# Performance work log

Measured on AMD Instinct MI355X. Metric: run time of the kernel, lower is better.

The kernel has to match this reference:

```python
import jax, jax.numpy as jnp
import numpy as np

T, B, E, H = 2048, 2, 1024, 16
DH = E // H
SCALE = DH ** -0.5
NEG = jnp.finfo(jnp.float32).min


def setup_inputs() -> dict:
    key = jax.random.key(0)
    ks = jax.random.split(key, 10)
    s = 0.02
    query = jax.random.normal(ks[0], (T, B, E), dtype=jnp.float32)
    key_padding_mask = jax.random.randint(ks[1], (B, T), 0, 2).astype(bool)
    # causal additive mask, broadcastable over (bsz, heads, tgt, src)
    causal = jnp.triu(jnp.ones((T, T), dtype=bool), k=1)
    attn_mask = jnp.where(causal, NEG, 0.0).astype(jnp.float32)[None, None]
    Wq = jax.random.normal(ks[2], (E, E), jnp.float32) * s
    bq = jax.random.normal(ks[3], (E,), jnp.float32) * s
    Wk = jax.random.normal(ks[4], (E, E), jnp.float32) * s
    bk = jax.random.normal(ks[5], (E,), jnp.float32) * s
    Wv = jax.random.normal(ks[6], (E, E), jnp.float32) * s
    bv = jax.random.normal(ks[7], (E,), jnp.float32) * s
    Wo = jax.random.normal(ks[8], (E, E), jnp.float32) * s
    bo = jax.random.normal(ks[9], (E,), jnp.float32) * s
    return {"query": query, "key_padding_mask": key_padding_mask, "attn_mask": attn_mask,
            "Wq": Wq, "bq": bq, "Wk": Wk, "bk": bk, "Wv": Wv, "bv": bv, "Wo": Wo, "bo": bo}


def _heads(x):
    # [T, B, E] -> [B, H, T, DH]
    return x.reshape(T, B, H, DH).transpose(1, 2, 0, 3)


def reference(query, key_padding_mask, attn_mask, Wq, bq, Wk, bk, Wv, bv, Wo, bo):
    # projections (torch Linear: x @ W.T + b); q scaled as in module
    q = _heads((query @ Wq.T + bq) * SCALE)          # [B,H,T,DH]
    k = _heads(query @ Wk.T + bk)                    # [B,H,S,DH] (self-attn: S=T)
    v = _heads(query @ Wv.T + bv)
    scores = jnp.einsum('bhtd,bhsd->bhts', q, k)     # [B,H,T,S]
    scores = scores + attn_mask                      # additive causal mask
    # key_padding_mask True -> masked_fill with dtype min
    scores = jnp.where(key_padding_mask[:, None, None, :], NEG, scores)
    probs = jax.nn.softmax(scores, axis=-1)
    ctx = jnp.einsum('bhts,bhsd->bhtd', probs, v)    # [B,H,T,DH]
    ctx = ctx.transpose(2, 0, 1, 3).reshape(T, B, E) # back to [T,B,E]
    return ctx @ Wo.T + bo
```

## Files before the change

kernel.cpp:

```cpp
#include <hip/hip_runtime.h>
#include <hip/hip_bf16.h>
#include <stdint.h>

typedef unsigned short u16;
typedef uint32_t u32;
typedef unsigned long long u64;
typedef __attribute__((ext_vector_type(8))) short bf16x8;
typedef __attribute__((ext_vector_type(4))) float f32x4;
typedef __attribute__((ext_vector_type(16))) float f32x16;
typedef __attribute__((ext_vector_type(4))) u32 u32x4;

#define T_SEQ 2048

__device__ __forceinline__ float bf2f(u16 u) {
  union { u32 i; float f; } v; v.i = ((u32)u) << 16; return v.f;
}
__device__ __forceinline__ u16 f2bf(float f) {
  union { float f; u32 i; } v; v.f = f;
  u32 u = v.i;
  return (u16)((u + 0x7fffu + ((u >> 16) & 1u)) >> 16);
}

#if __has_builtin(__builtin_amdgcn_exp2f)
#define EXP2F(x) __builtin_amdgcn_exp2f(x)
#else
#define EXP2F(x) exp2f(x)
#endif

__device__ __forceinline__ u32 permpack(float lo, float hi) {
#if __has_builtin(__builtin_amdgcn_perm)
  return __builtin_amdgcn_perm(__float_as_uint(hi), __float_as_uint(lo), 0x07060302u);
#else
  return (__float_as_uint(hi) & 0xFFFF0000u) | (__float_as_uint(lo) >> 16);
#endif
}

__device__ __forceinline__ void gload_lds16(const void* g, void* l) {
  __builtin_amdgcn_global_load_lds(
      (const __attribute__((address_space(1))) void*)g,
      (__attribute__((address_space(3))) void*)l, 16, 0, 0);
}

__global__ __launch_bounds__(256) void cvt_kernel(const float* __restrict__ src,
                                                  u16* __restrict__ dst, int n) {
  int i = (blockIdx.x * 256 + threadIdx.x) * 4;
  if (i + 3 < n) {
    const float4 v = *(const float4*)(src + i);
    ushort4 o;
    o.x = f2bf(v.x); o.y = f2bf(v.y); o.z = f2bf(v.z); o.w = f2bf(v.w);
    *(ushort4*)(dst + i) = o;
  }
}

__global__ __launch_bounds__(256) void cvt4_kernel(
    const float* __restrict__ s0, const float* __restrict__ s1,
    const float* __restrict__ s2, const float* __restrict__ s3,
    u16* __restrict__ dst) {
  const int z = blockIdx.y;
  const float* src = (z == 0) ? s0 : (z == 1) ? s1 : (z == 2) ? s2 : s3;
  int i = (blockIdx.x * 256 + threadIdx.x) * 4;
  const float4 v = *(const float4*)(src + i);
  ushort4 o;
  o.x = f2bf(v.x); o.y = f2bf(v.y); o.z = f2bf(v.z); o.w = f2bf(v.w);
  *(ushort4*)(dst + (size_t)z * 1048576 + i) = o;
}

__device__ __forceinline__ void gemm_core_128x128(
    f32x4 acc[2][4], const u16* __restrict__ A, const u16* __restrict__ Bw,
    int bm, int bn, u16* As, u16* Bs)
{
  const int tid = threadIdx.x;
  const int w = tid >> 6, lane = tid & 63, g = lane >> 4, c = lane & 15;
  const int wr = (w & 3) * 32, wc = (w >> 2) * 64;
  for (int k0 = 0; k0 < 1024; k0 += 64) {
    __syncthreads();
    #pragma unroll
    for (int is = 0; is < 2; ++is) {
      int o = (is*8 + w)*1024 + lane*16;
      int row = o >> 7, c16 = (o >> 4) & 7;
      gload_lds16(A + (size_t)(bm*128 + row)*1024 + k0 + (c16 ^ (row & 7))*8,
                  (char*)As + (is*8 + w)*1024);
    }
    #pragma unroll
    for (int is = 0; is < 2; ++is) {
      int o = (is*8 + w)*1024 + lane*16;
      int row = o >> 7, c16 = (o >> 4) & 7;
      gload_lds16(Bw + (size_t)(bn*128 + row)*1024 + k0 + (c16 ^ (row & 7))*8,
                  (char*)Bs + (is*8 + w)*1024);
    }
    __syncthreads();
    bf16x8 af[2][2], bfr[4][2];
    #pragma unroll
    for (int mf = 0; mf < 2; ++mf)
      #pragma unroll
      for (int kc = 0; kc < 2; ++kc) {
        int row = wr + mf*16 + c;
        int colb = kc*64 + g*16;
        af[mf][kc] = *(const bf16x8*)((const char*)As + row*128 + (colb ^ ((row & 7) << 4)));
      }
    #pragma unroll
    for (int nf = 0; nf < 4; ++nf)
      #pragma unroll
      for (int kc = 0; kc < 2; ++kc) {
        int row = wc + nf*16 + c;
        int colb = kc*64 + g*16;
        bfr[nf][kc] = *(const bf16x8*)((const char*)Bs + row*128 + (colb ^ ((row & 7) << 4)));
      }
    #pragma unroll
    for (int mf = 0; mf < 2; ++mf)
      #pragma unroll
      for (int nf = 0; nf < 4; ++nf)
        #pragma unroll
        for (int kc = 0; kc < 2; ++kc)
          acc[mf][nf] = __builtin_amdgcn_mfma_f32_16x16x32_bf16(
              af[mf][kc], bfr[nf][kc], acc[mf][nf], 0, 0, 0);
  }
}

__global__ __launch_bounds__(512, 2) void gemm_qkv(
    const u16* __restrict__ Abf, const u16* __restrict__ Wbf,
    const float* __restrict__ bq, const float* __restrict__ bk,
    const float* __restrict__ bv, u16* __restrict__ qkvh)
{
  __shared__ __align__(16) u16 As[128*64];
  __shared__ __align__(16) u16 Bs[128*64];
  f32x4 acc[2][4];
  #pragma unroll
  for (int mf = 0; mf < 2; ++mf)
    #pragma unroll
    for (int nf = 0; nf < 4; ++nf) acc[mf][nf] = (f32x4){0.f,0.f,0.f,0.f};
  const int z = blockIdx.z;
  gemm_core_128x128(acc, Abf, Wbf + (size_t)z*1048576, blockIdx.x, blockIdx.y, As, Bs);
  const float* bias = (z == 0) ? bq : (z == 1) ? bk : bv;
  const float scl = (z == 0) ? 0.18033688011112043f : 1.0f;
  u16* dst = qkvh + (size_t)z * 4194304;
  const int tid = threadIdx.x, w = tid >> 6, lane = tid & 63, g = lane >> 4, c = lane & 15;
  const int wr = (w & 3) * 32, wc = (w >> 2) * 64;
  #pragma unroll
  for (int mf = 0; mf < 2; ++mf)
    #pragma unroll
    for (int nf = 0; nf < 4; ++nf) {
      int col = blockIdx.y*128 + wc + nf*16 + c;
      float bcol = bias[col];
      int h = col >> 6, d = col & 63;
      #pragma unroll
      for (int r = 0; r < 4; ++r) {
        int row = blockIdx.x*128 + wr + mf*16 + g*4 + r;
        int t = row >> 1, bb = row & 1;
        float v = (acc[mf][nf][r] + bcol) * scl;
        dst[(size_t)(bb*16 + h)*131072 + (size_t)t*64 + d] = f2bf(v);
      }
    }
}

__global__ __launch_bounds__(512, 2) void gemm_out(
    const u16* __restrict__ ctx2, const u16* __restrict__ Wobf,
    const float* __restrict__ bo, float* __restrict__ out)
{
  __shared__ __align__(16) u16 As[128*64];
  __shared__ __align__(16) u16 Bs[128*64];
  f32x4 acc[2][4];
  #pragma unroll
  for (int mf = 0; mf < 2; ++mf)
    #pragma unroll
    for (int nf = 0; nf < 4; ++nf) acc[mf][nf] = (f32x4){0.f,0.f,0.f,0.f};
  gemm_core_128x128(acc, ctx2, Wobf, blockIdx.x, blockIdx.y, As, Bs);
  const int tid = threadIdx.x, w = tid >> 6, lane = tid & 63, g = lane >> 4, c = lane & 15;
  const int wr = (w & 3) * 32, wc = (w >> 2) * 64;
  #pragma unroll
  for (int mf = 0; mf < 2; ++mf)
    #pragma unroll
    for (int nf = 0; nf < 4; ++nf) {
      int col = blockIdx.y*128 + wc + nf*16 + c;
      float bcol = bo[col];
      #pragma unroll
      for (int r = 0; r < 4; ++r) {
        int row = blockIdx.x*128 + wr + mf*16 + g*4 + r;
        out[(size_t)row*1024 + col] = acc[mf][nf][r] + bcol;
      }
    }
}

__global__ __launch_bounds__(256) void vtrans_kernel(const u16* __restrict__ Vh,
                                                     u16* __restrict__ Vt,
                                                     float* __restrict__ vs) {
  __shared__ u16 tile[64][72];
  const int bh = blockIdx.x >> 5, tc = blockIdx.x & 31;
  const int t0 = tc * 64;
  const int tid = threadIdx.x;
  {
    const int tl = tid >> 2, d0 = (tid & 3) * 16;
    const u16* src = Vh + (size_t)bh*131072 + (size_t)(t0 + tl)*64 + d0;
    bf16x8 a = *(const bf16x8*)src;
    bf16x8 b2 = *(const bf16x8*)(src + 8);
    #pragma unroll
    for (int j = 0; j < 8; ++j) {
      tile[d0 + j][tl] = (u16)a[j];
      tile[d0 + 8 + j][tl] = (u16)b2[j];
    }
  }
  __syncthreads();
  {
    const int d = tid >> 2, tq = (tid & 3) * 16;
    bf16x8 o0, o1;
    float s = 0.f;
    #pragma unroll
    for (int j = 0; j < 8; ++j) {
      u16 x0 = tile[d][tq + j], x1 = tile[d][tq + 8 + j];
      o0[j] = (short)x0; o1[j] = (short)x1;
      s += bf2f(x0) + bf2f(x1);
    }
    u16* dst = Vt + (size_t)bh*131072 + (size_t)d*2048 + t0 + tq;
    *(bf16x8*)dst = o0;
    *(bf16x8*)(dst + 8) = o1;
    s += __shfl_xor(s, 1, 64);
    s += __shfl_xor(s, 2, 64);
    if ((tid & 3) == 0) atomicAdd(&vs[bh*64 + d], s);
  }
}

#define ZERO16 (f32x16){0.f,0.f,0.f,0.f,0.f,0.f,0.f,0.f,0.f,0.f,0.f,0.f,0.f,0.f,0.f,0.f}
#define NEGINF (-__builtin_inff())

__global__ __launch_bounds__(64, 2) void flash_attn(
    const u16* __restrict__ Qh, const u16* __restrict__ Kh,
    const u16* __restrict__ Vt, const int* __restrict__ kpm,
    const float* __restrict__ vsum, u16* __restrict__ ctx2,
    u16* __restrict__ pctx, float* __restrict__ pml)
{
  const int lane = threadIdx.x;
  const int l31 = lane & 31, hi = lane >> 5;

  const int id = blockIdx.x;
  const int xcd = id & 7, rest = id >> 3;
  const int bh = xcd * 4 + (rest & 3);
  const int pp = rest >> 2;
  int qt, ch, NS;
  if (pp < 32) { qt = pp; ch = 0; NS = 1; }
  else { int uu = pp - 32; qt = 32 + (uu >> 1); ch = uu & 1; NS = 2; }
  const int b = bh >> 4, h = bh & 15;
  const int q0 = qt * 32;
  const size_t hbase = (size_t)bh * 131072;
  const int nt = (qt >> 1) + 1;
  int lo, hicap;
  if (NS == 1) { lo = 0; hicap = nt; }
  else { int h1 = nt >> 1; lo = ch ? h1 : 0; hicap = ch ? nt : h1; }
  const int q = q0 + l31;

  bf16x8 qfrag[4];
  #pragma unroll
  for (int kt = 0; kt < 4; ++kt)
    qfrag[kt] = *(const bf16x8*)(Qh + hbase + (size_t)q*64 + kt*16 + hi*8);

  bf16x8 kreg[2][4];
  #pragma unroll
  for (int sub = 0; sub < 2; ++sub)
    #pragma unroll
    for (int kt = 0; kt < 4; ++kt)
      kreg[sub][kt] = *(const bf16x8*)(Kh + hbase + (size_t)(lo*64 + sub*32 + l31)*64 + kt*16 + hi*8);

  int kpmv_cur = kpm[b*T_SEQ + lo*64 + lane];
  int kpmv_nxt = 0;

  float mrow = NEGINF, lrow = 0.f;
  f32x16 cacc0 = ZERO16, cacc1 = ZERO16;

  for (int t = lo; t < hicap; ++t) {
    const int s0 = t * 64;
    const bool notLast = (t + 1 < hicap);
    const bool diag = (t == nt - 1);

    bf16x8 vf[2][4];
    #pragma unroll
    for (int db = 0; db < 2; ++db)
      #pragma unroll
      for (int ks = 0; ks < 4; ++ks)
        vf[db][ks] = *(const bf16x8*)(Vt + hbase + (size_t)(db*32 + l31)*2048 + s0 + ks*16 + hi*8);

    f32x16 st0 = ZERO16, st1 = ZERO16;
    __builtin_amdgcn_s_setprio(1);
    #pragma unroll
    for (int kt = 0; kt < 4; ++kt) {
      st0 = __builtin_amdgcn_mfma_f32_32x32x16_bf16(kreg[0][kt], qfrag[kt], st0, 0, 0, 0);
      st1 = __builtin_amdgcn_mfma_f32_32x32x16_bf16(kreg[1][kt], qfrag[kt], st1, 0, 0, 0);
    }
    __builtin_amdgcn_s_setprio(0);

    if (notLast) {
      #pragma unroll
      for (int sub = 0; sub < 2; ++sub)
        #pragma unroll
        for (int kt = 0; kt < 4; ++kt)
          kreg[sub][kt] = *(const bf16x8*)(Kh + hbase + (size_t)(s0 + 64 + sub*32 + l31)*64 + kt*16 + hi*8);
      kpmv_nxt = kpm[b*T_SEQ + s0 + 64 + lane];
    }

    {
      const u64 mask = __ballot(kpmv_cur != 0);
      const u32 m0 = (u32)mask, m1 = (u32)(mask >> 32);
      const u64 m4 = mask >> 4;
      const u32 m4l = (u32)m4, m4h = (u32)(m4 >> 32);
      const u32 w0 = hi ? m4l : m0;
      const u32 w1 = hi ? m4h : m1;
      const int lim = q - s0 - 4*hi;
      #pragma unroll
      for (int m = 0; m < 4; ++m) {
        u32 nib0 = (w0 >> (m*8)) & 15u;
        u32 nib1 = (w1 >> (m*8)) & 15u;
        if (diag) {
          int t0c = lim - m*8;       int c0 = min(max(t0c + 1, 0), 4);
          int t1c = lim - 32 - m*8;  int c1 = min(max(t1c + 1, 0), 4);
          nib0 |= (0xFu << c0) & 0xFu;
          nib1 |= (0xFu << c1) & 0xFu;
        }
        #pragma unroll
        for (int r = 0; r < 4; ++r) {
          if ((nib0 >> r) & 1) st0[m*4 + r] = NEGINF;
          if ((nib1 >> r) & 1) st1[m*4 + r] = NEGINF;
        }
      }
      float t8[8];
      #pragma unroll
      for (int i = 0; i < 8; ++i)
        t8[i] = fmaxf(fmaxf(st0[i], st0[i+8]), fmaxf(st1[i], st1[i+8]));
      float t4a = fmaxf(t8[0], t8[4]), t4b = fmaxf(t8[1], t8[5]);
      float t4c = fmaxf(t8[2], t8[6]), t4d = fmaxf(t8[3], t8[7]);
      float rm = fmaxf(fmaxf(t4a, t4b), fmaxf(t4c, t4d));
      rm = fmaxf(rm, __shfl_xor(rm, 32, 64));

      const bool need = (rm > mrow + 8.f) || (mrow < -1e30f);
      if (__any(need)) {
        const float mn = fmaxf(mrow, rm);
        const float sc = (mn < -1e30f) ? 1.f : EXP2F(mrow - mn);
        mrow = mn;
        lrow *= sc;
        #pragma unroll
        for (int i = 0; i < 16; ++i) { cacc0[i] *= sc; cacc1[i] *= sc; }
      }
      const bool dead = (mrow < -1e30f);
      float a0 = 0.f, a1 = 0.f, a2 = 0.f, a3 = 0.f;
      #pragma unroll
      for (int i = 0; i < 16; i += 4) {
        float p0 = dead ? 0.f : EXP2F(st0[i+0] - mrow); st0[i+0] = p0; a0 += p0;
        float p1 = dead ? 0.f : EXP2F(st0[i+1] - mrow); st0[i+1] = p1; a1 += p1;
        float p2 = dead ? 0.f : EXP2F(st0[i+2] - mrow); st0[i+2] = p2; a2 += p2;
        float p3 = dead ? 0.f : EXP2F(st0[i+3] - mrow); st0[i+3] = p3; a3 += p3;
      }
      #pragma unroll
      for (int i = 0; i < 16; i += 4) {
        float p0 = dead ? 0.f : EXP2F(st1[i+0] - mrow); st1[i+0] = p0; a0 += p0;
        float p1 = dead ? 0.f : EXP2F(st1[i+1] - mrow); st1[i+1] = p1; a1 += p1;
        float p2 = dead ? 0.f : EXP2F(st1[i+2] - mrow); st1[i+2] = p2; a2 += p2;
        float p3 = dead ? 0.f : EXP2F(st1[i+3] - mrow); st1[i+3] = p3; a3 += p3;
      }
      float ps = (a0 + a1) + (a2 + a3);
      ps += __shfl_xor(ps, 32, 64);
      lrow += ps;
    }

    u32 pk[8][2];
    #pragma unroll
    for (int m = 0; m < 4; ++m) {
      pk[m][0]   = permpack(st0[m*4+0], st0[m*4+1]);
      pk[m][1]   = permpack(st0[m*4+2], st0[m*4+3]);
      pk[4+m][0] = permpack(st1[m*4+0], st1[m*4+1]);
      pk[4+m][1] = permpack(st1[m*4+2], st1[m*4+3]);
    }
    bf16x8 pf[4];
    #pragma unroll
    for (int ks = 0; ks < 4; ++ks) {
      u32 own0 = pk[2*ks][0],   own1 = pk[2*ks][1];
      u32 oth0 = pk[2*ks+1][0], oth1 = pk[2*ks+1][1];
      u32 r0 = __shfl_xor(hi ? own0 : oth0, 32, 64);
      u32 r1 = __shfl_xor(hi ? own1 : oth1, 32, 64);
      u32 w0 = hi ? r0 : own0;
      u32 w1 = hi ? r1 : own1;
      u32 w2 = hi ? oth0 : r0;
      u32 w3 = hi ? oth1 : r1;
      u32x4 wv = {w0, w1, w2, w3};
      pf[ks] = __builtin_bit_cast(bf16x8, wv);
    }

    __builtin_amdgcn_s_setprio(1);
    #pragma unroll
    for (int ks = 0; ks < 4; ++ks)
      cacc0 = __builtin_amdgcn_mfma_f32_32x32x16_bf16(vf[0][ks], pf[ks], cacc0, 0, 0, 0);
    #pragma unroll
    for (int ks = 0; ks < 4; ++ks)
      cacc1 = __builtin_amdgcn_mfma_f32_32x32x16_bf16(vf[1][ks], pf[ks], cacc1, 0, 0, 0);
    __builtin_amdgcn_s_setprio(0);

    kpmv_cur = kpmv_nxt;
  }

  if (NS == 1) {
    const bool dead = (lrow == 0.f);
    const float rl = dead ? 0.f : 1.f / lrow;
    #pragma unroll
    for (int subd = 0; subd < 2; ++subd) {
      #pragma unroll
      for (int m = 0; m < 4; ++m) {
        const int d0 = subd*32 + hi*4 + m*8;
        float v0 = (subd ? cacc1[m*4+0] : cacc0[m*4+0]) * rl;
        float v1 = (subd ? cacc1[m*4+1] : cacc0[m*4+1]) * rl;
        float v2 = (subd ? cacc1[m*4+2] : cacc0[m*4+2]) * rl;
        float v3 = (subd ? cacc1[m*4+3] : cacc0[m*4+3]) * rl;
        if (dead) {
          const float* vs = vsum + bh*64 + d0;
          v0 = vs[0] * (1.0f/2048.0f);
          v1 = vs[1] * (1.0f/2048.0f);
          v2 = vs[2] * (1.0f/2048.0f);
          v3 = vs[3] * (1.0f/2048.0f);
        }
        ushort4 o;
        o.x = f2bf(v0); o.y = f2bf(v1); o.z = f2bf(v2); o.w = f2bf(v3);
        *(ushort4*)(ctx2 + (size_t)(q*2 + b)*1024 + h*64 + d0) = o;
      }
    }
  } else {
    const int slot = ((bh << 5) + (qt - 32))*2 + ch;
    u16* pc = pctx + (size_t)slot*2048 + (size_t)l31*64;
    #pragma unroll
    for (int subd = 0; subd < 2; ++subd) {
      #pragma unroll
      for (int m = 0; m < 4; ++m) {
        const int d0 = subd*32 + hi*4 + m*8;
        const f32x16& cc = subd ? cacc1 : cacc0;
        ushort4 o;
        o.x = f2bf(cc[m*4+0]); o.y = f2bf(cc[m*4+1]);
        o.z = f2bf(cc[m*4+2]); o.w = f2bf(cc[m*4+3]);
        *(ushort4*)(pc + d0) = o;
      }
    }
    if (!hi) {
      float2 ml; ml.x = mrow; ml.y = lrow;
      *(float2*)(pml + (size_t)slot*64 + l31*2) = ml;
    }
  }
}

__global__ __launch_bounds__(64) void combine_kernel(
    const u16* __restrict__ pctx, const float* __restrict__ pml,
    const float* __restrict__ vsum, u16* __restrict__ ctx2)
{
  const int qtm = blockIdx.x, bh = blockIdx.y;
  const int qt = 32 + qtm;
  const int b = bh >> 4, h = bh & 15;
  const int lane = threadIdx.x;
  const int qr = lane >> 1, d0 = (lane & 1) * 32;
  const int slot0 = ((bh << 5) + qtm)*2;
  const float* ml0 = pml + (size_t)slot0*64 + qr*2;
  const float* ml1 = pml + (size_t)(slot0+1)*64 + qr*2;
  const float m1 = ml0[0], l1 = ml0[1];
  const float m2 = ml1[0], l2 = ml1[1];
  const float ms = fmaxf(m1, m2);
  bool dead = (ms == NEGINF);
  const float w1 = dead ? 0.f : EXP2F(m1 - ms);
  const float w2 = dead ? 0.f : EXP2F(m2 - ms);
  const float lt = w1*l1 + w2*l2;
  dead = dead || (lt == 0.f);
  const float rl = dead ? 0.f : 1.f / lt;
  const u16* c1 = pctx + ((size_t)slot0*32 + qr)*64 + d0;
  const u16* c2 = pctx + ((size_t)(slot0+1)*32 + qr)*64 + d0;
  const int qrow = qt*32 + qr;
  u16* dst = ctx2 + (size_t)(qrow*2 + b)*1024 + h*64 + d0;
  #pragma unroll
  for (int g2 = 0; g2 < 4; ++g2) {
    bf16x8 a = *(const bf16x8*)(c1 + g2*8);
    bf16x8 bb = *(const bf16x8*)(c2 + g2*8);
    bf16x8 o;
    #pragma unroll
    for (int j = 0; j < 8; ++j) {
      float v = (w1*bf2f((u16)a[j]) + w2*bf2f((u16)bb[j])) * rl;
      if (dead) v = vsum[bh*64 + d0 + g2*8 + j] * (1.0f/2048.0f);
      o[j] = (short)f2bf(v);
    }
    *(bf16x8*)(dst + g2*8) = o;
  }
}

extern "C" void kernel_launch(void* const* d_in, const int* in_sizes, int n_in,
                              void* d_out, int out_size, void* d_ws, size_t ws_size,
                              hipStream_t stream) {
  const float* query = (const float*)d_in[0];
  const int*   kpm   = (const int*)d_in[1];
  const float* Wq = (const float*)d_in[3];
  const float* bq = (const float*)d_in[4];
  const float* Wk = (const float*)d_in[5];
  const float* bk = (const float*)d_in[6];
  const float* Wv = (const float*)d_in[7];
  const float* bv = (const float*)d_in[8];
  const float* Wo = (const float*)d_in[9];
  const float* bo = (const float*)d_in[10];

  char* ws = (char*)d_ws;
  u16*   qbf  = (u16*)(ws);
  u16*   Vt   = (u16*)(ws);
  u16*   wbf  = (u16*)(ws + 8388608);
  u16*   qkvh = (u16*)(ws + 16777216);
  u16*   pctx = (u16*)(ws + 33554432);
  u16*   ctx2 = (u16*)(ws + 41943040);
  float* vsum = (float*)(ws + 50331648);
  float* pml  = (float*)(ws + 50339840);

  cvt_kernel<<<dim3(4096), 256, 0, stream>>>(query, qbf, 4194304);
  cvt4_kernel<<<dim3(1024, 4), 256, 0, stream>>>(Wq, Wk, Wv, Wo, wbf);

  hipMemsetAsync(vsum, 0, 2048 * sizeof(float), stream);

  gemm_qkv<<<dim3(32, 8, 3), 512, 0, stream>>>(qbf, wbf, bq, bk, bv, qkvh);
  vtrans_kernel<<<dim3(1024), 256, 0, stream>>>(qkvh + 2*4194304, Vt, vsum);
  flash_attn<<<dim3(3072), 64, 0, stream>>>(qkvh, qkvh + 1*4194304,
                                            Vt, kpm, vsum, ctx2, pctx, pml);
  combine_kernel<<<dim3(32, 32), 64, 0, stream>>>(pctx, pml, vsum, ctx2);
  gemm_out<<<dim3(32, 8), 512, 0, stream>>>(ctx2, wbf + 3*1048576, bo, (float*)d_out);
}
```

Before: 152.2 us.

## Share K/V tiles via double-buffered LDS across two query waves in flash attention

Flash attention now runs two 32-row query waves per 128-thread block covering a 64-row query tile. K and V tiles are loaded into XOR-swizzled, double-buffered LDS with direct global-to-LDS loads, one wave loading K and the other V, so both waves share each tile instead of each fetching it from global memory. The work-to-block mapping is reordered so longer diagonal tiles are scheduled first. Separately, the QKV GEMM drops the z grid dimension and treats the three weight matrices as one wide N, deriving bias, scale and destination per column. The cost is LDS use and a block barrier every iteration.

```diff
diff --git a/kernel.cpp b/kernel.cpp
--- a/kernel.cpp
+++ b/kernel.cpp
@@ -129,11 +129,7 @@
   for (int mf = 0; mf < 2; ++mf)
     #pragma unroll
     for (int nf = 0; nf < 4; ++nf) acc[mf][nf] = (f32x4){0.f,0.f,0.f,0.f};
-  const int z = blockIdx.z;
-  gemm_core_128x128(acc, Abf, Wbf + (size_t)z*1048576, blockIdx.x, blockIdx.y, As, Bs);
-  const float* bias = (z == 0) ? bq : (z == 1) ? bk : bv;
-  const float scl = (z == 0) ? 0.18033688011112043f : 1.0f;
-  u16* dst = qkvh + (size_t)z * 4194304;
+  gemm_core_128x128(acc, Abf, Wbf, blockIdx.x, blockIdx.y, As, Bs);
   const int tid = threadIdx.x, w = tid >> 6, lane = tid & 63, g = lane >> 4, c = lane & 15;
   const int wr = (w & 3) * 32, wc = (w >> 2) * 64;
   #pragma unroll
@@ -141,8 +137,12 @@
     #pragma unroll
     for (int nf = 0; nf < 4; ++nf) {
       int col = blockIdx.y*128 + wc + nf*16 + c;
-      float bcol = bias[col];
-      int h = col >> 6, d = col & 63;
+      int z = col >> 10, colz = col & 1023;
+      const float* bias = (z == 0) ? bq : (z == 1) ? bk : bv;
+      float bcol = bias[colz];
+      float scl = (z == 0) ? 0.18033688011112043f : 1.0f;
+      int h = colz >> 6, d = colz & 63;
+      u16* dst = qkvh + (size_t)z * 4194304;
       #pragma unroll
       for (int r = 0; r < 4; ++r) {
         int row = blockIdx.x*128 + wr + mf*16 + g*4 + r;
@@ -222,60 +222,104 @@
 #define ZERO16 (f32x16){0.f,0.f,0.f,0.f,0.f,0.f,0.f,0.f,0.f,0.f,0.f,0.f,0.f,0.f,0.f,0.f}
 #define NEGINF (-__builtin_inff())
 
-__global__ __launch_bounds__(64, 2) void flash_attn(
+__global__ __launch_bounds__(128, 2) void flash_attn(
     const u16* __restrict__ Qh, const u16* __restrict__ Kh,
     const u16* __restrict__ Vt, const int* __restrict__ kpm,
     const float* __restrict__ vsum, u16* __restrict__ ctx2,
     u16* __restrict__ pctx, float* __restrict__ pml)
 {
-  const int lane = threadIdx.x;
+  __shared__ __align__(16) u16 Kl[2][4096];
+  __shared__ __align__(16) u16 Vl[2][4096];
+
+  const int tid = threadIdx.x;
+  const int w = tid >> 6, lane = tid & 63;
   const int l31 = lane & 31, hi = lane >> 5;
 
   const int id = blockIdx.x;
   const int xcd = id & 7, rest = id >> 3;
   const int bh = xcd * 4 + (rest & 3);
-  const int pp = rest >> 2;
-  int qt, ch, NS;
-  if (pp < 32) { qt = pp; ch = 0; NS = 1; }
-  else { int uu = pp - 32; qt = 32 + (uu >> 1); ch = uu & 1; NS = 2; }
+  const int pr = rest >> 2;
+  int k, ch, NS;
+  if (pr < 32) { k = 31 - (pr >> 1); ch = pr & 1; NS = 2; }
+  else         { k = 47 - pr;        ch = 0;      NS = 1; }
+  const int nt = k + 1;
   const int b = bh >> 4, h = bh & 15;
-  const int q0 = qt * 32;
   const size_t hbase = (size_t)bh * 131072;
-  const int nt = (qt >> 1) + 1;
   int lo, hicap;
   if (NS == 1) { lo = 0; hicap = nt; }
   else { int h1 = nt >> 1; lo = ch ? h1 : 0; hicap = ch ? nt : h1; }
-  const int q = q0 + l31;
+  const int q = k*64 + w*32 + l31;
 
   bf16x8 qfrag[4];
   #pragma unroll
   for (int kt = 0; kt < 4; ++kt)
     qfrag[kt] = *(const bf16x8*)(Qh + hbase + (size_t)q*64 + kt*16 + hi*8);
 
-  bf16x8 kreg[2][4];
-  #pragma unroll
-  for (int sub = 0; sub < 2; ++sub)
-    #pragma unroll
-    for (int kt = 0; kt < 4; ++kt)
-      kreg[sub][kt] = *(const bf16x8*)(Kh + hbase + (size_t)(lo*64 + sub*32 + l31)*64 + kt*16 + hi*8);
-
+  {
+    const int s0t = lo * 64;
+    if (w == 0) {
+      #pragma unroll
+      for (int is = 0; is < 8; ++is) {
+        int o = is*1024 + lane*16;
+        int row = o >> 7, c16 = (o >> 4) & 7;
+        gload_lds16(Kh + hbase + (size_t)(s0t + row)*64 + (c16 ^ (row & 7))*8,
+                    (char*)Kl[0] + is*1024);
+      }
+    } else {
+      #pragma unroll
+      for (int is = 0; is < 8; ++is) {
+        int o = is*1024 + lane*16;
+        int row = o >> 7, c16 = (o >> 4) & 7;
+        gload_lds16(Vt + hbase + (size_t)row*2048 + s0t + (c16 ^ (row & 7))*8,
+                    (char*)Vl[0] + is*1024);
+      }
+    }
+  }
   int kpmv_cur = kpm[b*T_SEQ + lo*64 + lane];
   int kpmv_nxt = 0;
+  __syncthreads();
 
   float mrow = NEGINF, lrow = 0.f;
   f32x16 cacc0 = ZERO16, cacc1 = ZERO16;
 
   for (int t = lo; t < hicap; ++t) {
+    const int cur = (t - lo) & 1, nxt = cur ^ 1;
     const int s0 = t * 64;
     const bool notLast = (t + 1 < hicap);
     const bool diag = (t == nt - 1);
 
-    bf16x8 vf[2][4];
-    #pragma unroll
-    for (int db = 0; db < 2; ++db)
-      #pragma unroll
-      for (int ks = 0; ks < 4; ++ks)
-        vf[db][ks] = *(const bf16x8*)(Vt + hbase + (size_t)(db*32 + l31)*2048 + s0 + ks*16 + hi*8);
+    if (notLast) {
+      const int s0n = s0 + 64;
+      if (w == 0) {
+        #pragma unroll
+        for (int is = 0; is < 8; ++is) {
+          int o = is*1024 + lane*16;
+          int row = o >> 7, c16 = (o >> 4) & 7;
+          gload_lds16(Kh + hbase + (size_t)(s0n + row)*64 + (c16 ^ (row & 7))*8,
+                      (char*)Kl[nxt] + is*1024);
+        }
+      } else {
+        #pragma unroll
+        for (int is = 0; is < 8; ++is) {
+          int o = is*1024 + lane*16;
+          int row = o >> 7, c16 = (o >> 4) & 7;
+          gload_lds16(Vt + hbase + (size_t)row*2048 + s0n + (c16 ^ (row & 7))*8,
+                      (char*)Vl[nxt] + is*1024);
+        }
+      }
+      kpmv_nxt = kpm[b*T_SEQ + s0n + lane];
+    }
+
+    bf16x8 kreg[2][4], vf[2][4];
+    #pragma unroll
+    for (int sub = 0; sub < 2; ++sub)
+      #pragma unroll
+      for (int kt = 0; kt < 4; ++kt) {
+        int row = sub*32 + l31;
+        int colb = kt*32 + hi*16;
+        kreg[sub][kt] = *(const bf16x8*)((const char*)Kl[cur] + row*128 + (colb ^ ((row & 7) << 4)));
+        vf[sub][kt]   = *(const bf16x8*)((const char*)Vl[cur] + row*128 + (colb ^ ((row & 7) << 4)));
+      }
 
     f32x16 st0 = ZERO16, st1 = ZERO16;
     __builtin_amdgcn_s_setprio(1);
@@ -285,15 +329,6 @@
       st1 = __builtin_amdgcn_mfma_f32_32x32x16_bf16(kreg[1][kt], qfrag[kt], st1, 0, 0, 0);
     }
     __builtin_amdgcn_s_setprio(0);
-
-    if (notLast) {
-      #pragma unroll
-      for (int sub = 0; sub < 2; ++sub)
-        #pragma unroll
-        for (int kt = 0; kt < 4; ++kt)
-          kreg[sub][kt] = *(const bf16x8*)(Kh + hbase + (size_t)(s0 + 64 + sub*32 + l31)*64 + kt*16 + hi*8);
-      kpmv_nxt = kpm[b*T_SEQ + s0 + 64 + lane];
-    }
 
     {
       const u64 mask = __ballot(kpmv_cur != 0);
@@ -391,8 +426,10 @@
     __builtin_amdgcn_s_setprio(0);
 
     kpmv_cur = kpmv_nxt;
-  }
-
+    if (notLast) __syncthreads();
+  }
+
+  const int qt32 = 2*k + w;
   if (NS == 1) {
     const bool dead = (lrow == 0.f);
     const float rl = dead ? 0.f : 1.f / lrow;
@@ -418,7 +455,7 @@
       }
     }
   } else {
-    const int slot = ((bh << 5) + (qt - 32))*2 + ch;
+    const int slot = ((bh << 5) + (qt32 - 32))*2 + ch;
     u16* pc = pctx + (size_t)slot*2048 + (size_t)l31*64;
     #pragma unroll
     for (int subd = 0; subd < 2; ++subd) {
@@ -508,10 +545,10 @@
 
   hipMemsetAsync(vsum, 0, 2048 * sizeof(float), stream);
 
-  gemm_qkv<<<dim3(32, 8, 3), 512, 0, stream>>>(qbf, wbf, bq, bk, bv, qkvh);
+  gemm_qkv<<<dim3(32, 24), 512, 0, stream>>>(qbf, wbf, bq, bk, bv, qkvh);
   vtrans_kernel<<<dim3(1024), 256, 0, stream>>>(qkvh + 2*4194304, Vt, vsum);
-  flash_attn<<<dim3(3072), 64, 0, stream>>>(qkvh, qkvh + 1*4194304,
-                                            Vt, kpm, vsum, ctx2, pctx, pml);
+  flash_attn<<<dim3(1536), 128, 0, stream>>>(qkvh, qkvh + 1*4194304,
+                                             Vt, kpm, vsum, ctx2, pctx, pml);
   combine_kernel<<<dim3(32, 32), 64, 0, stream>>>(pctx, pml, vsum, ctx2);
   gemm_out<<<dim3(32, 8), 512, 0, stream>>>(ctx2, wbf + 3*1048576, bo, (float*)d_out);
 }
```

Result: faster. 133.7 us (-12.2%).
